# Performance work log

Measured on AMD Instinct MI355X. Metric: run time of the kernel, lower is better.

The kernel has to match this reference:

```python
import jax, jax.numpy as jnp
import numpy as np

T, B, D = 256, 16, 512          # time, batch, intermediate_dim (GRU is seq-first)
HR = 256                         # router_dim
EXPERT_DIMS = [0, 128, 256, 512]
NUM_TASKS = 4
COST_EXP = 1.0
BN_EPS = 1e-5


def _gru(x, w_ih, w_hh, b_ih, b_hh):
    """PyTorch-semantics GRU over axis 0. x: (T, ..., D) -> (T, ..., H).
    Works batched (T,B,D) or unbatched (N,D) exactly like nn.GRU."""
    H = w_hh.shape[1]
    gi = x @ w_ih.T + b_ih            # (T, ..., 3H) input projections, done once
    h0 = jnp.zeros(x.shape[1:-1] + (H,), x.dtype)

    def step(h, gi_t):
        gh = h @ w_hh.T + b_hh
        i_r, i_z, i_n = jnp.split(gi_t, 3, axis=-1)
        h_r, h_z, h_n = jnp.split(gh, 3, axis=-1)
        r = jax.nn.sigmoid(i_r + h_r)
        z = jax.nn.sigmoid(i_z + h_z)
        n = jnp.tanh(i_n + r * h_n)
        h_new = (1.0 - z) * n + z * h
        return h_new, h_new

    _, ys = jax.lax.scan(step, h0, gi)
    return ys


def setup_inputs() -> dict:
    key = jax.random.key(0)
    ks = iter(jax.random.split(key, 64))

    def p(shape, fan_in):
        return (jax.random.normal(next(ks), shape, jnp.float32) / np.sqrt(fan_in)).astype(jnp.float32)

    inp = {
        'x': jax.random.normal(next(ks), (T, B, D), jnp.float32),
        'task_ids': jax.random.randint(next(ks), (T, B), 0, NUM_TASKS),
        # router params
        'router_w_ih': p((3 * HR, D), D),
        'router_w_hh': p((3 * HR, HR), HR),
        'router_b_ih': jnp.zeros((3 * HR,), jnp.float32),
        'router_b_hh': jnp.zeros((3 * HR,), jnp.float32),
        'router_out_w': p((len(EXPERT_DIMS), HR), HR),
        'router_out_b': jnp.zeros((len(EXPERT_DIMS),), jnp.float32),
    }
    for i, H in enumerate(EXPERT_DIMS):
        if H == 0:
            continue
        inp[f'e{i}_w_ih'] = p((3 * H, D), D)
        inp[f'e{i}_w_hh'] = p((3 * H, H), H)
        inp[f'e{i}_b_ih'] = jnp.zeros((3 * H,), jnp.float32)
        inp[f'e{i}_b_hh'] = jnp.zeros((3 * H,), jnp.float32)
        inp[f'e{i}_bn_g'] = jnp.ones((H,), jnp.float32)
        inp[f'e{i}_bn_b'] = jnp.zeros((H,), jnp.float32)
        inp[f'e{i}_out_w'] = p((D, H), H)
        inp[f'e{i}_out_b'] = jnp.zeros((D,), jnp.float32)
    return inp


def reference(x, task_ids,
              router_w_ih, router_w_hh, router_b_ih, router_b_hh,
              router_out_w, router_out_b,
              e1_w_ih, e1_w_hh, e1_b_ih, e1_b_hh, e1_bn_g, e1_bn_b, e1_out_w, e1_out_b,
              e2_w_ih, e2_w_hh, e2_b_ih, e2_b_hh, e2_bn_g, e2_bn_b, e2_out_w, e2_out_b,
              e3_w_ih, e3_w_hh, e3_b_ih, e3_b_hh, e3_bn_g, e3_bn_b, e3_out_w, e3_out_b):
    E = len(EXPERT_DIMS)
    # ---- router: GRU -> ReLU -> Linear -> softmax ----
    hs = _gru(x, router_w_ih, router_w_hh, router_b_ih, router_b_hh)   # (T,B,HR)
    logits = jax.nn.relu(hs) @ router_out_w.T + router_out_b           # (T,B,E)
    raw = jax.nn.softmax(logits, axis=-1)                              # raw_router_output
    # no dropout configured -> router_output == raw, all experts active

    # ---- task expert usage losses ----
    costs = jnp.asarray([d ** COST_EXP for d in EXPERT_DIMS], logits.dtype)
    eul = jnp.einsum('tbe,e->tb', raw, costs).reshape(-1)
    tflat = task_ids.reshape(-1)
    sums = jax.ops.segment_sum(eul, tflat, num_segments=NUM_TASKS)
    cnts = jax.ops.segment_sum(jnp.ones_like(eul), tflat, num_segments=NUM_TASKS)
    task_losses = sums / cnts                                           # (NUM_TASKS,)

    # ---- experts: each sees the flat (N,D) tokens as ONE unbatched GRU sequence ----
    flat_x = x.reshape(-1, D)                                           # (N,D)
    gates = raw.reshape(-1, E)                                          # (N,E)
    out = gates[:, 0:1] * flat_x                                        # expert 0 = identity

    eps = [(e1_w_ih, e1_w_hh, e1_b_ih, e1_b_hh, e1_bn_g, e1_bn_b, e1_out_w, e1_out_b),
           (e2_w_ih, e2_w_hh, e2_b_ih, e2_b_hh, e2_bn_g, e2_bn_b, e2_out_w, e2_out_b),
           (e3_w_ih, e3_w_hh, e3_b_ih, e3_b_hh, e3_bn_g, e3_bn_b, e3_out_w, e3_out_b)]
    for i, (w_ih, w_hh, b_ih, b_hh, g, b, ow, ob) in enumerate(eps, start=1):
        h = _gru(flat_x, w_ih, w_hh, b_ih, b_hh)                        # (N,H) unbatched seq
        mu = h.mean(0)
        var = ((h - mu) ** 2).mean(0)                                   # biased var (train-mode BN)
        hn = (h - mu) / jnp.sqrt(var + BN_EPS) * g + b
        eo = jax.nn.relu(hn) @ ow.T + ob                                # (N,D)
        out = out + gates[:, i:i + 1] * eo

    final_output = out.reshape(T, B, D)
    return final_output, raw, task_losses
```

## Files before the change

kernel.cpp:

```cpp
#include <hip/hip_runtime.h>
#include <math.h>

constexpr int TT = 256, BB = 16, DD = 512;
constexpr int NTOK = 4096;
constexpr int RTOT = 3456;
constexpr int E1OFF = 768, E2OFF = 1152, E3OFF = 1920;

constexpr size_t OFF_TSUM = 0;
constexpr size_t OFF_TCNT = 16;
constexpr size_t OFF_CNT  = 32;
constexpr size_t ZBYTES   = 64;
constexpr size_t OFF_GI   = 4096;
constexpr size_t OFF_HS   = OFF_GI  + (size_t)NTOK*RTOT*4;
constexpr size_t OFF_HA3  = OFF_HS  + (size_t)NTOK*256*4;
constexpr size_t OFF_HA2  = OFF_HA3 + (size_t)NTOK*512*4;
constexpr size_t OFF_HA1  = OFF_HA2 + (size_t)NTOK*256*4;
constexpr size_t OFF_AP   = OFF_HA1 + (size_t)NTOK*128*4;
constexpr size_t OFF_MU   = OFF_AP  + (size_t)NTOK*896*4;
constexpr size_t OFF_RSTD = OFF_MU  + 896*4;
constexpr size_t POISON_BYTES = (size_t)NTOK*(256+512+256+128)*4;

__device__ __forceinline__ bool is_poison(float v) {
  return __float_as_uint(v) == 0xAAAAAAAAu;
}

__global__ __launch_bounds__(256) void gemm1_kernel(
    const float* __restrict__ X,
    const float* __restrict__ wR, const float* __restrict__ w1,
    const float* __restrict__ w2, const float* __restrict__ w3,
    const float* __restrict__ bR, const float* __restrict__ b1,
    const float* __restrict__ b2, const float* __restrict__ b3,
    float* __restrict__ GI)
{
  __shared__ float At[32*64];
  __shared__ float Bt[32*64];
  const int n0 = blockIdx.x * 64;
  const int r0 = blockIdx.y * 64;
  const float* W; const float* bias; int rs;
  if (r0 < 768)       { W = wR; bias = bR; rs = 0; }
  else if (r0 < 1152) { W = w1; bias = b1; rs = 768; }
  else if (r0 < 1920) { W = w2; bias = b2; rs = 1152; }
  else                { W = w3; bias = b3; rs = 1920; }
  const int lr0 = r0 - rs;
  const int tid = threadIdx.x;
  const int lm = tid & 63, lk4 = tid >> 6;
  const int tx = tid & 15, ty = tid >> 4;
  float acc[4][4];
#pragma unroll
  for (int i = 0; i < 4; ++i)
#pragma unroll
    for (int q = 0; q < 4; ++q) acc[i][q] = 0.f;

  for (int kb = 0; kb < 512; kb += 32) {
    const float4 a0 = *(const float4*)(X + (size_t)(n0+lm)*512 + kb + lk4*8);
    const float4 a1 = *(const float4*)(X + (size_t)(n0+lm)*512 + kb + lk4*8 + 4);
    const float4 c0 = *(const float4*)(W + (size_t)(lr0+lm)*512 + kb + lk4*8);
    const float4 c1 = *(const float4*)(W + (size_t)(lr0+lm)*512 + kb + lk4*8 + 4);
    __syncthreads();
    At[(lk4*8+0)*64+lm]=a0.x; At[(lk4*8+1)*64+lm]=a0.y; At[(lk4*8+2)*64+lm]=a0.z; At[(lk4*8+3)*64+lm]=a0.w;
    At[(lk4*8+4)*64+lm]=a1.x; At[(lk4*8+5)*64+lm]=a1.y; At[(lk4*8+6)*64+lm]=a1.z; At[(lk4*8+7)*64+lm]=a1.w;
    Bt[(lk4*8+0)*64+lm]=c0.x; Bt[(lk4*8+1)*64+lm]=c0.y; Bt[(lk4*8+2)*64+lm]=c0.z; Bt[(lk4*8+3)*64+lm]=c0.w;
    Bt[(lk4*8+4)*64+lm]=c1.x; Bt[(lk4*8+5)*64+lm]=c1.y; Bt[(lk4*8+6)*64+lm]=c1.z; Bt[(lk4*8+7)*64+lm]=c1.w;
    __syncthreads();
#pragma unroll
    for (int k = 0; k < 32; ++k) {
      const float4 av = *(const float4*)&At[k*64 + ty*4];
      const float4 bv = *(const float4*)&Bt[k*64 + tx*4];
      acc[0][0]=fmaf(av.x,bv.x,acc[0][0]); acc[0][1]=fmaf(av.x,bv.y,acc[0][1]); acc[0][2]=fmaf(av.x,bv.z,acc[0][2]); acc[0][3]=fmaf(av.x,bv.w,acc[0][3]);
      acc[1][0]=fmaf(av.y,bv.x,acc[1][0]); acc[1][1]=fmaf(av.y,bv.y,acc[1][1]); acc[1][2]=fmaf(av.y,bv.z,acc[1][2]); acc[1][3]=fmaf(av.y,bv.w,acc[1][3]);
      acc[2][0]=fmaf(av.z,bv.x,acc[2][0]); acc[2][1]=fmaf(av.z,bv.y,acc[2][1]); acc[2][2]=fmaf(av.z,bv.z,acc[2][2]); acc[2][3]=fmaf(av.z,bv.w,acc[2][3]);
      acc[3][0]=fmaf(av.w,bv.x,acc[3][0]); acc[3][1]=fmaf(av.w,bv.y,acc[3][1]); acc[3][2]=fmaf(av.w,bv.z,acc[3][2]); acc[3][3]=fmaf(av.w,bv.w,acc[3][3]);
    }
  }
  const float4 bb = *(const float4*)(bias + lr0 + tx*4);
#pragma unroll
  for (int i = 0; i < 4; ++i) {
    float4 o;
    o.x = acc[i][0] + bb.x; o.y = acc[i][1] + bb.y; o.z = acc[i][2] + bb.z; o.w = acc[i][3] + bb.w;
    *(float4*)(GI + (size_t)(n0+ty*4+i)*RTOT + r0 + tx*4) = o;
  }
}

struct ScanArgs {
  const float* GI;
  const float* rwhh; const float* rbhh; float* hs;
  const float* w1; const float* b1; float* ha1;
  const float* w2; const float* b2; float* ha2;
  const float* w3; const float* b3; float* ha3;
  int* cnt;
};

template<int H, int OPW>
__device__ void expert_scan(const float* __restrict__ GIe, const float* __restrict__ whh,
                            const float* __restrict__ bhh, float* __restrict__ hall,
                            float* __restrict__ sm, int wg)
{
  constexpr int KCN = 512 / OPW;
  constexpr bool SINGLE = (OPW == H);
  const int tid = threadIdx.x;
  const int j = tid / KCN, kc = tid % KCN;
  const int jg = wg * OPW + j;

  float4 wr[8], wz[8], wn[8];
#pragma unroll
  for (int i4 = 0; i4 < 8; ++i4) {
    const int kk = kc * 32 + ((i4 + kc) & 7) * 4;
    wr[i4] = *(const float4*)(whh + (size_t)jg * H + kk);
    wz[i4] = *(const float4*)(whh + (size_t)(H + jg) * H + kk);
    wn[i4] = *(const float4*)(whh + (size_t)(2*H + jg) * H + kk);
  }
  float gbr = 0.f, gbz = 0.f, gbn = 0.f;
  float gr0 = 0.f, gz0 = 0.f, gn0 = 0.f, gr1 = 0.f, gz1 = 0.f, gn1 = 0.f;
  if (kc == 0) {
    gbr = bhh[jg]; gbz = bhh[H + jg]; gbn = bhh[2*H + jg];
    gr0 = GIe[jg]; gz0 = GIe[H + jg]; gn0 = GIe[2*H + jg];
    const float* g1 = GIe + RTOT;
    gr1 = g1[jg]; gz1 = g1[H + jg]; gn1 = g1[2*H + jg];
  }
  if (SINGLE) {
    if (tid < H) sm[tid] = 0.f;
    __syncthreads();
  }
  for (int t = 0; t < NTOK; ++t) {
    float gr2 = 0.f, gz2 = 0.f, gn2 = 0.f;
    if (kc == 0 && t + 2 < NTOK) {
      const float* g = GIe + (size_t)(t + 2) * RTOT;
      gr2 = g[jg]; gz2 = g[H + jg]; gn2 = g[2*H + jg];
    }
    const float* hbuf;
    if (SINGLE) {
      hbuf = sm + (size_t)(t & 1) * H;
    } else {
      float val = 0.f;
      if (tid < H && t > 0) {
        const volatile float* p = (const volatile float*)(hall + (size_t)(t - 1) * H + tid);
        val = *p;
        while (is_poison(val)) val = *p;
      }
      __syncthreads();
      if (tid < H) sm[tid] = val;
      __syncthreads();
      hbuf = sm;
    }
    float pr = 0.f, pz = 0.f, pn = 0.f;
#pragma unroll
    for (int i4 = 0; i4 < 8; ++i4) {
      const float4 h4 = *(const float4*)(hbuf + kc * 32 + ((i4 + kc) & 7) * 4);
      pr = fmaf(wr[i4].x, h4.x, pr); pr = fmaf(wr[i4].y, h4.y, pr);
      pr = fmaf(wr[i4].z, h4.z, pr); pr = fmaf(wr[i4].w, h4.w, pr);
      pz = fmaf(wz[i4].x, h4.x, pz); pz = fmaf(wz[i4].y, h4.y, pz);
      pz = fmaf(wz[i4].z, h4.z, pz); pz = fmaf(wz[i4].w, h4.w, pz);
      pn = fmaf(wn[i4].x, h4.x, pn); pn = fmaf(wn[i4].y, h4.y, pn);
      pn = fmaf(wn[i4].z, h4.z, pn); pn = fmaf(wn[i4].w, h4.w, pn);
    }
#pragma unroll
    for (int off = KCN / 2; off; off >>= 1) {
      pr += __shfl_down(pr, off); pz += __shfl_down(pz, off); pn += __shfl_down(pn, off);
    }
    if (kc == 0) {
      const float hprev = hbuf[jg];
      const float rg = 1.f / (1.f + expf(-(gr0 + gbr + pr)));
      const float zg = 1.f / (1.f + expf(-(gz0 + gbz + pz)));
      const float nn = tanhf(gn0 + rg * (pn + gbn));
      const float hn = (1.f - zg) * nn + zg * hprev;
      if (SINGLE) {
        sm[(size_t)((t + 1) & 1) * H + jg] = hn;
        hall[(size_t)t * H + jg] = hn;
      } else {
        *(volatile float*)(hall + (size_t)t * H + jg) = hn;
      }
    }
    if (SINGLE) __syncthreads();
    gr0 = gr1; gz0 = gz1; gn0 = gn1;
    gr1 = gr2; gz1 = gz2; gn1 = gn2;
  }
}

__device__ void router_scan(const float* __restrict__ GI, const float* __restrict__ whh,
                            const float* __restrict__ bhh, float* __restrict__ hs,
                            float* __restrict__ sm, int wg)
{
  float* hsmB = sm;
  float* pbuf = sm + 16 * 260;
  const int tid = threadIdx.x;
  const int j = tid >> 4, kc = tid & 15;
  const int jg = wg * 32 + j;
  float4 wr4[4], wz4[4], wn4[4];
#pragma unroll
  for (int i4 = 0; i4 < 4; ++i4) {
    const int kk = kc * 16 + ((i4 + kc) & 3) * 4;
    wr4[i4] = *(const float4*)(whh + (size_t)jg * 256 + kk);
    wz4[i4] = *(const float4*)(whh + (size_t)(256 + jg) * 256 + kk);
    wn4[i4] = *(const float4*)(whh + (size_t)(512 + jg) * 256 + kk);
  }
  const int b2 = tid >> 5, j2 = tid & 31;
  const int jg2 = wg * 32 + j2;
  const float gbr = bhh[jg2], gbz = bhh[256 + jg2], gbn = bhh[512 + jg2];
  float gr0, gz0, gn0, gr1, gz1, gn1;
  { const float* g = GI + (size_t)b2 * RTOT;        gr0 = g[jg2]; gz0 = g[256 + jg2]; gn0 = g[512 + jg2]; }
  { const float* g = GI + (size_t)(16 + b2) * RTOT; gr1 = g[jg2]; gz1 = g[256 + jg2]; gn1 = g[512 + jg2]; }
  const int pb = tid >> 5, pk = (tid & 31) * 8;

  for (int t = 0; t < TT; ++t) {
    float gr2 = 0.f, gz2 = 0.f, gn2 = 0.f;
    if (t + 2 < TT) {
      const float* g = GI + (size_t)((t + 2) * 16 + b2) * RTOT;
      gr2 = g[jg2]; gz2 = g[256 + jg2]; gn2 = g[512 + jg2];
    }
    float v[8];
    if (t == 0) {
#pragma unroll
      for (int u = 0; u < 8; ++u) v[u] = 0.f;
    } else {
      const volatile float* q = (const volatile float*)(hs + (size_t)(t - 1) * 4096 + tid * 8);
#pragma unroll
      for (int u = 0; u < 8; ++u) v[u] = q[u];
      bool bad = true;
      while (bad) {
        bad = false;
#pragma unroll
        for (int u = 0; u < 8; ++u)
          if (is_poison(v[u])) { v[u] = q[u]; bad = true; }
      }
    }
    __syncthreads();
    *(float4*)(hsmB + pb * 260 + pk)     = make_float4(v[0], v[1], v[2], v[3]);
    *(float4*)(hsmB + pb * 260 + pk + 4) = make_float4(v[4], v[5], v[6], v[7]);
    __syncthreads();
    float ar[16], az[16], an[16];
#pragma unroll
    for (int b = 0; b < 16; ++b) { ar[b] = 0.f; az[b] = 0.f; an[b] = 0.f; }
#pragma unroll
    for (int i4 = 0; i4 < 4; ++i4) {
      const int col = kc * 16 + ((i4 + kc) & 3) * 4;
#pragma unroll
      for (int b = 0; b < 16; ++b) {
        const float4 h4 = *(const float4*)(hsmB + b * 260 + col);
        ar[b] = fmaf(wr4[i4].x, h4.x, ar[b]); ar[b] = fmaf(wr4[i4].y, h4.y, ar[b]);
        ar[b] = fmaf(wr4[i4].z, h4.z, ar[b]); ar[b] = fmaf(wr4[i4].w, h4.w, ar[b]);
        az[b] = fmaf(wz4[i4].x, h4.x, az[b]); az[b] = fmaf(wz4[i4].y, h4.y, az[b]);
        az[b] = fmaf(wz4[i4].z, h4.z, az[b]); az[b] = fmaf(wz4[i4].w, h4.w, az[b]);
        an[b] = fmaf(wn4[i4].x, h4.x, an[b]); an[b] = fmaf(wn4[i4].y, h4.y, an[b]);
        an[b] = fmaf(wn4[i4].z, h4.z, an[b]); an[b] = fmaf(wn4[i4].w, h4.w, an[b]);
      }
    }
#pragma unroll
    for (int off = 8; off; off >>= 1) {
#pragma unroll
      for (int b = 0; b < 16; ++b) {
        ar[b] += __shfl_down(ar[b], off);
        az[b] += __shfl_down(az[b], off);
        an[b] += __shfl_down(an[b], off);
      }
    }
    if (kc == 0) {
#pragma unroll
      for (int b = 0; b < 16; ++b) {
        pbuf[(b * 32 + j) * 3 + 0] = ar[b];
        pbuf[(b * 32 + j) * 3 + 1] = az[b];
        pbuf[(b * 32 + j) * 3 + 2] = an[b];
      }
    }
    __syncthreads();
    const float pr = pbuf[(b2 * 32 + j2) * 3 + 0];
    const float pz = pbuf[(b2 * 32 + j2) * 3 + 1];
    const float pn = pbuf[(b2 * 32 + j2) * 3 + 2];
    const float hprev = hsmB[b2 * 260 + jg2];
    const float rg = 1.f / (1.f + expf(-(gr0 + gbr + pr)));
    const float zg = 1.f / (1.f + expf(-(gz0 + gbz + pz)));
    const float nn = tanhf(gn0 + rg * (pn + gbn));
    const float hn = (1.f - zg) * nn + zg * hprev;
    *(volatile float*)(hs + (size_t)t * 4096 + b2 * 256 + jg2) = hn;
    gr0 = gr1; gz0 = gz1; gn0 = gn1;
    gr1 = gr2; gz1 = gz2; gn1 = gn2;
  }
}

__global__ __launch_bounds__(512, 1) void scan_kernel(ScanArgs A)
{
  __shared__ float sm[16 * 260 + 1536];
  __shared__ int role_s[2];
  if (threadIdx.x == 0) {
    unsigned x;
    asm volatile("s_getreg_b32 %0, hwreg(HW_REG_XCC_ID)" : "=s"(x));
    const int xcd = (int)(x & 7u);
    role_s[0] = xcd;
    role_s[1] = atomicAdd(A.cnt + xcd, 1);
  }
  __syncthreads();
  const int xcd = role_s[0], r = role_s[1];
  if (xcd == 0)      { if (r < 16) expert_scan<512, 32>(A.GI + E3OFF, A.w3, A.b3, A.ha3, sm, r); }
  else if (xcd == 1) { if (r < 8)  router_scan(A.GI, A.rwhh, A.rbhh, A.hs, sm, r); }
  else if (xcd == 2) { if (r < 4)  expert_scan<256, 64>(A.GI + E2OFF, A.w2, A.b2, A.ha2, sm, r); }
  else if (xcd == 3) { if (r < 1)  expert_scan<128,128>(A.GI + E1OFF, A.w1, A.b1, A.ha1, sm, r); }
}

__global__ __launch_bounds__(256) void router_out_kernel(
    const float* __restrict__ hs, const float* __restrict__ ow, const float* __restrict__ ob,
    const int* __restrict__ tids, float* __restrict__ raw_out,
    float* __restrict__ tsum, float* __restrict__ tcnt)
{
  const int tid = threadIdx.x;
  const int lane = tid & 63, w = tid >> 6;
  const int n = blockIdx.x * 4 + w;
  float s0 = 0.f, s1 = 0.f, s2 = 0.f, s3 = 0.f;
#pragma unroll
  for (int q = 0; q < 4; ++q) {
    const int jj = lane + q * 64;
    float h = hs[(size_t)n * 256 + jj];
    h = h > 0.f ? h : 0.f;
    s0 = fmaf(h, ow[jj], s0);
    s1 = fmaf(h, ow[256 + jj], s1);
    s2 = fmaf(h, ow[512 + jj], s2);
    s3 = fmaf(h, ow[768 + jj], s3);
  }
  for (int off = 32; off; off >>= 1) {
    s0 += __shfl_xor(s0, off); s1 += __shfl_xor(s1, off);
    s2 += __shfl_xor(s2, off); s3 += __shfl_xor(s3, off);
  }
  if (lane == 0) {
    const float l0 = s0 + ob[0], l1 = s1 + ob[1], l2 = s2 + ob[2], l3 = s3 + ob[3];
    const float m = fmaxf(fmaxf(l0, l1), fmaxf(l2, l3));
    const float e0 = expf(l0 - m), e1 = expf(l1 - m), e2 = expf(l2 - m), e3 = expf(l3 - m);
    const float inv = 1.f / (e0 + e1 + e2 + e3);
    float4 rv; rv.x = e0 * inv; rv.y = e1 * inv; rv.z = e2 * inv; rv.w = e3 * inv;
    *(float4*)(raw_out + (size_t)n * 4) = rv;
    const float eul = rv.y * 128.f + rv.z * 256.f + rv.w * 512.f;
    const int tk = tids[n];
    atomicAdd(&tsum[tk], eul);
    atomicAdd(&tcnt[tk], 1.f);
  }
}

__global__ __launch_bounds__(256) void bn_stats_kernel(
    const float* __restrict__ h1, const float* __restrict__ h2, const float* __restrict__ h3,
    float* __restrict__ mu, float* __restrict__ rstd)
{
  const int c = blockIdx.x;
  const float* hp; int He, hc;
  if (c < 128)      { hp = h1; He = 128; hc = c; }
  else if (c < 384) { hp = h2; He = 256; hc = c - 128; }
  else              { hp = h3; He = 512; hc = c - 384; }
  float s = 0.f, s2 = 0.f;
  for (int r = threadIdx.x; r < NTOK; r += 256) {
    const float v = hp[(size_t)r * He + hc];
    s += v; s2 = fmaf(v, v, s2);
  }
  for (int off = 32; off; off >>= 1) { s += __shfl_xor(s, off); s2 += __shfl_xor(s2, off); }
  __shared__ float red[8];
  const int lane = threadIdx.x & 63, w = threadIdx.x >> 6;
  if (lane == 0) { red[w] = s; red[4 + w] = s2; }
  __syncthreads();
  if (threadIdx.x == 0) {
    const float S = red[0] + red[1] + red[2] + red[3];
    const float S2 = red[4] + red[5] + red[6] + red[7];
    const float m = S * (1.f / 4096.f);
    float v = S2 * (1.f / 4096.f) - m * m;
    v = v > 0.f ? v : 0.f;
    mu[c] = m;
    rstd[c] = 1.f / sqrtf(v + 1e-5f);
  }
}

__global__ __launch_bounds__(256) void aprime_kernel(
    const float* __restrict__ h1, const float* __restrict__ h2, const float* __restrict__ h3,
    const float* __restrict__ g1, const float* __restrict__ be1,
    const float* __restrict__ g2, const float* __restrict__ be2,
    const float* __restrict__ g3, const float* __restrict__ be3,
    const float* __restrict__ mu, const float* __restrict__ rstd,
    const float* __restrict__ raw, float* __restrict__ Ap,
    const float* __restrict__ tsum, const float* __restrict__ tcnt, float* __restrict__ tl_out)
{
  if (blockIdx.x == 4096) {
    if (threadIdx.x < 4) tl_out[threadIdx.x] = tsum[threadIdx.x] / tcnt[threadIdx.x];
    return;
  }
  const int n = blockIdx.x;
  for (int c = threadIdx.x; c < 896; c += 256) {
    const float* hp; const float* gg; const float* bb; int He, hc, e;
    if (c < 128)      { hp = h1; gg = g1; bb = be1; He = 128; hc = c;       e = 1; }
    else if (c < 384) { hp = h2; gg = g2; bb = be2; He = 256; hc = c - 128; e = 2; }
    else              { hp = h3; gg = g3; bb = be3; He = 512; hc = c - 384; e = 3; }
    const float h = hp[(size_t)n * He + hc];
    float v = (h - mu[c]) * rstd[c] * gg[hc] + bb[hc];
    v = v > 0.f ? v : 0.f;
    Ap[(size_t)n * 896 + c] = raw[(size_t)n * 4 + e] * v;
  }
}

__global__ __launch_bounds__(256) void out_gemm_kernel(
    const float* __restrict__ Ap,
    const float* __restrict__ ow1, const float* __restrict__ ow2, const float* __restrict__ ow3,
    const float* __restrict__ ob1, const float* __restrict__ ob2, const float* __restrict__ ob3,
    const float* __restrict__ X, const float* __restrict__ raw, float* __restrict__ out)
{
  __shared__ float At[32*64];
  __shared__ float Bt[32*64];
  const int n0 = blockIdx.x * 64;
  const int d0 = blockIdx.y * 64;
  const int tid = threadIdx.x;
  const int lm = tid & 63, lk4 = tid >> 6;
  const int tx = tid & 15, ty = tid >> 4;
  float acc[4][4];
#pragma unroll
  for (int i = 0; i < 4; ++i)
#pragma unroll
    for (int q = 0; q < 4; ++q) acc[i][q] = 0.f;

  for (int kb = 0; kb < 896; kb += 32) {
    const float* W; int He, ko;
    if (kb < 128)      { W = ow1; He = 128; ko = 0; }
    else if (kb < 384) { W = ow2; He = 256; ko = 128; }
    else               { W = ow3; He = 512; ko = 384; }
    const float4 a0 = *(const float4*)(Ap + (size_t)(n0+lm)*896 + kb + lk4*8);
    const float4 a1 = *(const float4*)(Ap + (size_t)(n0+lm)*896 + kb + lk4*8 + 4);
    const float4 c0 = *(const float4*)(W + (size_t)(d0+lm)*He + (kb - ko) + lk4*8);
    const float4 c1 = *(const float4*)(W + (size_t)(d0+lm)*He + (kb - ko) + lk4*8 + 4);
    __syncthreads();
    At[(lk4*8+0)*64+lm]=a0.x; At[(lk4*8+1)*64+lm]=a0.y; At[(lk4*8+2)*64+lm]=a0.z; At[(lk4*8+3)*64+lm]=a0.w;
    At[(lk4*8+4)*64+lm]=a1.x; At[(lk4*8+5)*64+lm]=a1.y; At[(lk4*8+6)*64+lm]=a1.z; At[(lk4*8+7)*64+lm]=a1.w;
    Bt[(lk4*8+0)*64+lm]=c0.x; Bt[(lk4*8+1)*64+lm]=c0.y; Bt[(lk4*8+2)*64+lm]=c0.z; Bt[(lk4*8+3)*64+lm]=c0.w;
    Bt[(lk4*8+4)*64+lm]=c1.x; Bt[(lk4*8+5)*64+lm]=c1.y; Bt[(lk4*8+6)*64+lm]=c1.z; Bt[(lk4*8+7)*64+lm]=c1.w;
    __syncthreads();
#pragma unroll
    for (int k = 0; k < 32; ++k) {
      const float4 av = *(const float4*)&At[k*64 + ty*4];
      const float4 bv = *(const float4*)&Bt[k*64 + tx*4];
      acc[0][0]=fmaf(av.x,bv.x,acc[0][0]); acc[0][1]=fmaf(av.x,bv.y,acc[0][1]); acc[0][2]=fmaf(av.x,bv.z,acc[0][2]); acc[0][3]=fmaf(av.x,bv.w,acc[0][3]);
      acc[1][0]=fmaf(av.y,bv.x,acc[1][0]); acc[1][1]=fmaf(av.y,bv.y,acc[1][1]); acc[1][2]=fmaf(av.y,bv.z,acc[1][2]); acc[1][3]=fmaf(av.y,bv.w,acc[1][3]);
      acc[2][0]=fmaf(av.z,bv.x,acc[2][0]); acc[2][1]=fmaf(av.z,bv.y,acc[2][1]); acc[2][2]=fmaf(av.z,bv.z,acc[2][2]); acc[2][3]=fmaf(av.z,bv.w,acc[2][3]);
      acc[3][0]=fmaf(av.w,bv.x,acc[3][0]); acc[3][1]=fmaf(av.w,bv.y,acc[3][1]); acc[3][2]=fmaf(av.w,bv.z,acc[3][2]); acc[3][3]=fmaf(av.w,bv.w,acc[3][3]);
    }
  }
#pragma unroll
  for (int i = 0; i < 4; ++i) {
    const int n = n0 + ty * 4 + i;
    const float4 g  = *(const float4*)(raw + (size_t)n * 4);
    const float4 xv = *(const float4*)(X + (size_t)n * 512 + d0 + tx * 4);
    const float4 o1 = *(const float4*)(ob1 + d0 + tx * 4);
    const float4 o2 = *(const float4*)(ob2 + d0 + tx * 4);
    const float4 o3 = *(const float4*)(ob3 + d0 + tx * 4);
    float4 o;
    o.x = acc[i][0] + g.x*xv.x + g.y*o1.x + g.z*o2.x + g.w*o3.x;
    o.y = acc[i][1] + g.x*xv.y + g.y*o1.y + g.z*o2.y + g.w*o3.y;
    o.z = acc[i][2] + g.x*xv.z + g.y*o1.z + g.z*o2.z + g.w*o3.z;
    o.w = acc[i][3] + g.x*xv.w + g.y*o1.w + g.z*o2.w + g.w*o3.w;
    *(float4*)(out + (size_t)n * 512 + d0 + tx * 4) = o;
  }
}

extern "C" void kernel_launch(void* const* d_in, const int* in_sizes, int n_in,
                              void* d_out, int out_size, void* d_ws, size_t ws_size,
                              hipStream_t stream) {
  const float* x    = (const float*)d_in[0];
  const int*   tids = (const int*)d_in[1];
  const float* rwih = (const float*)d_in[2];
  const float* rwhh = (const float*)d_in[3];
  const float* rbih = (const float*)d_in[4];
  const float* rbhh = (const float*)d_in[5];
  const float* row  = (const float*)d_in[6];
  const float* rob  = (const float*)d_in[7];
  const float* w1ih = (const float*)d_in[8];
  const float* w1hh = (const float*)d_in[9];
  const float* b1ih = (const float*)d_in[10];
  const float* b1hh = (const float*)d_in[11];
  const float* bn1g = (const float*)d_in[12];
  const float* bn1b = (const float*)d_in[13];
  const float* ow1  = (const float*)d_in[14];
  const float* ob1  = (const float*)d_in[15];
  const float* w2ih = (const float*)d_in[16];
  const float* w2hh = (const float*)d_in[17];
  const float* b2ih = (const float*)d_in[18];
  const float* b2hh = (const float*)d_in[19];
  const float* bn2g = (const float*)d_in[20];
  const float* bn2b = (const float*)d_in[21];
  const float* ow2  = (const float*)d_in[22];
  const float* ob2  = (const float*)d_in[23];
  const float* w3ih = (const float*)d_in[24];
  const float* w3hh = (const float*)d_in[25];
  const float* b3ih = (const float*)d_in[26];
  const float* b3hh = (const float*)d_in[27];
  const float* bn3g = (const float*)d_in[28];
  const float* bn3b = (const float*)d_in[29];
  const float* ow3  = (const float*)d_in[30];
  const float* ob3  = (const float*)d_in[31];

  char* ws = (char*)d_ws;
  float* tsum = (float*)(ws + OFF_TSUM);
  float* tcnt = (float*)(ws + OFF_TCNT);
  int*   cnt  = (int*)(ws + OFF_CNT);
  float* GI   = (float*)(ws + OFF_GI);
  float* hs   = (float*)(ws + OFF_HS);
  float* ha3  = (float*)(ws + OFF_HA3);
  float* ha2  = (float*)(ws + OFF_HA2);
  float* ha1  = (float*)(ws + OFF_HA1);
  float* Ap   = (float*)(ws + OFF_AP);
  float* mu   = (float*)(ws + OFF_MU);
  float* rstd = (float*)(ws + OFF_RSTD);

  float* outp = (float*)d_out;
  float* rawp = outp + (size_t)NTOK * DD;
  float* tlp  = rawp + (size_t)NTOK * 4;

  hipMemsetAsync(ws, 0, ZBYTES, stream);
  hipMemsetAsync(ws + OFF_HS, 0xAA, POISON_BYTES, stream);

  gemm1_kernel<<<dim3(64, 54), 256, 0, stream>>>(x, rwih, w1ih, w2ih, w3ih,
                                                 rbih, b1ih, b2ih, b3ih, GI);

  ScanArgs sa;
  sa.GI = GI; sa.rwhh = rwhh; sa.rbhh = rbhh; sa.hs = hs;
  sa.w1 = w1hh; sa.b1 = b1hh; sa.ha1 = ha1;
  sa.w2 = w2hh; sa.b2 = b2hh; sa.ha2 = ha2;
  sa.w3 = w3hh; sa.b3 = b3hh; sa.ha3 = ha3;
  sa.cnt = cnt;
  scan_kernel<<<dim3(320), dim3(512), 0, stream>>>(sa);

  router_out_kernel<<<dim3(1024), 256, 0, stream>>>(hs, row, rob, tids, rawp, tsum, tcnt);
  bn_stats_kernel<<<dim3(896), 256, 0, stream>>>(ha1, ha2, ha3, mu, rstd);
  aprime_kernel<<<dim3(4097), 256, 0, stream>>>(ha1, ha2, ha3, bn1g, bn1b, bn2g, bn2b,
                                                bn3g, bn3b, mu, rstd, rawp, Ap,
                                                tsum, tcnt, tlp);

  out_gemm_kernel<<<dim3(64, 8), 256, 0, stream>>>(Ap, ow1, ow2, ow3, ob1, ob2, ob3,
                                                   x, rawp, outp);
}
```

Baseline: 6.769 ms.

## Replace poison-flag scan sync with tagged 64-bit ring buffers and wider workgroup split

New measurement: 24.88 ms. +267.5%, slower.

```diff
diff --git a/kernel.cpp b/kernel.cpp
--- a/kernel.cpp
+++ b/kernel.cpp
@@ -6,11 +6,19 @@
 constexpr int RTOT = 3456;
 constexpr int E1OFF = 768, E2OFF = 1152, E3OFF = 1920;
 
-constexpr size_t OFF_TSUM = 0;
-constexpr size_t OFF_TCNT = 16;
-constexpr size_t OFF_CNT  = 32;
-constexpr size_t ZBYTES   = 64;
-constexpr size_t OFF_GI   = 4096;
+typedef unsigned long long ull;
+
+constexpr size_t OFF_TSUM  = 0;
+constexpr size_t OFF_TCNT  = 16;
+constexpr size_t OFF_CNT   = 32;
+constexpr size_t ZBYTES    = 64;
+constexpr size_t OFF_RINGR = 4096;
+constexpr size_t OFF_RING3 = OFF_RINGR + 8ull*4096*8;
+constexpr size_t OFF_RING2 = OFF_RING3 + 8ull*512*8;
+constexpr size_t OFF_RING1 = OFF_RING2 + 8ull*256*8;
+constexpr size_t RING_END  = OFF_RING1 + 8ull*128*8;
+constexpr size_t RING_BYTES = RING_END - OFF_RINGR;
+constexpr size_t OFF_GI   = 327680;
 constexpr size_t OFF_HS   = OFF_GI  + (size_t)NTOK*RTOT*4;
 constexpr size_t OFF_HA3  = OFF_HS  + (size_t)NTOK*256*4;
 constexpr size_t OFF_HA2  = OFF_HA3 + (size_t)NTOK*512*4;
@@ -18,11 +26,6 @@
 constexpr size_t OFF_AP   = OFF_HA1 + (size_t)NTOK*128*4;
 constexpr size_t OFF_MU   = OFF_AP  + (size_t)NTOK*896*4;
 constexpr size_t OFF_RSTD = OFF_MU  + 896*4;
-constexpr size_t POISON_BYTES = (size_t)NTOK*(256+512+256+128)*4;
-
-__device__ __forceinline__ bool is_poison(float v) {
-  return __float_as_uint(v) == 0xAAAAAAAAu;
-}
 
 __global__ __launch_bounds__(256) void gemm1_kernel(
     const float* __restrict__ X,
@@ -83,216 +86,223 @@
 
 struct ScanArgs {
   const float* GI;
-  const float* rwhh; const float* rbhh; float* hs;
-  const float* w1; const float* b1; float* ha1;
-  const float* w2; const float* b2; float* ha2;
-  const float* w3; const float* b3; float* ha3;
+  const float* rwhh; const float* rbhh; float* hs;  ull* ringR;
+  const float* w1;   const float* b1;   float* ha1; ull* ring1;
+  const float* w2;   const float* b2;   float* ha2; ull* ring2;
+  const float* w3;   const float* b3;   float* ha3; ull* ring3;
   int* cnt;
 };
 
 template<int H, int OPW>
 __device__ void expert_scan(const float* __restrict__ GIe, const float* __restrict__ whh,
                             const float* __restrict__ bhh, float* __restrict__ hall,
-                            float* __restrict__ sm, int wg)
+                            volatile ull* ring, int wg)
 {
   constexpr int KCN = 512 / OPW;
-  constexpr bool SINGLE = (OPW == H);
   const int tid = threadIdx.x;
   const int j = tid / KCN, kc = tid % KCN;
   const int jg = wg * OPW + j;
-
-  float4 wr[8], wz[8], wn[8];
-#pragma unroll
-  for (int i4 = 0; i4 < 8; ++i4) {
-    const int kk = kc * 32 + ((i4 + kc) & 7) * 4;
+  const int lane = tid & 63;
+  const int gbase = lane & ~(KCN - 1);
+
+  float4 wr[4], wz[4], wn[4];
+#pragma unroll
+  for (int i4 = 0; i4 < 4; ++i4) {
+    const int kk = kc * 16 + i4 * 4;
     wr[i4] = *(const float4*)(whh + (size_t)jg * H + kk);
     wz[i4] = *(const float4*)(whh + (size_t)(H + jg) * H + kk);
-    wn[i4] = *(const float4*)(whh + (size_t)(2*H + jg) * H + kk);
-  }
-  float gbr = 0.f, gbz = 0.f, gbn = 0.f;
-  float gr0 = 0.f, gz0 = 0.f, gn0 = 0.f, gr1 = 0.f, gz1 = 0.f, gn1 = 0.f;
-  if (kc == 0) {
-    gbr = bhh[jg]; gbz = bhh[H + jg]; gbn = bhh[2*H + jg];
-    gr0 = GIe[jg]; gz0 = GIe[H + jg]; gn0 = GIe[2*H + jg];
-    const float* g1 = GIe + RTOT;
-    gr1 = g1[jg]; gz1 = g1[H + jg]; gn1 = g1[2*H + jg];
-  }
-  if (SINGLE) {
-    if (tid < H) sm[tid] = 0.f;
-    __syncthreads();
-  }
+    wn[i4] = *(const float4*)(whh + (size_t)(2 * H + jg) * H + kk);
+  }
+  const float gbr = bhh[jg], gbz = bhh[H + jg], gbn = bhh[2 * H + jg];
+  float pgr, pgz, pgn;
+  { const float* g = GIe + (size_t)kc * RTOT;
+    pgr = __builtin_nontemporal_load(g + jg);
+    pgz = __builtin_nontemporal_load(g + H + jg);
+    pgn = __builtin_nontemporal_load(g + 2 * H + jg); }
+
   for (int t = 0; t < NTOK; ++t) {
-    float gr2 = 0.f, gz2 = 0.f, gn2 = 0.f;
-    if (kc == 0 && t + 2 < NTOK) {
-      const float* g = GIe + (size_t)(t + 2) * RTOT;
-      gr2 = g[jg]; gz2 = g[H + jg]; gn2 = g[2*H + jg];
-    }
-    const float* hbuf;
-    if (SINGLE) {
-      hbuf = sm + (size_t)(t & 1) * H;
-    } else {
-      float val = 0.f;
-      if (tid < H && t > 0) {
-        const volatile float* p = (const volatile float*)(hall + (size_t)(t - 1) * H + tid);
-        val = *p;
-        while (is_poison(val)) val = *p;
-      }
-      __syncthreads();
-      if (tid < H) sm[tid] = val;
-      __syncthreads();
-      hbuf = sm;
-    }
-    float pr = 0.f, pz = 0.f, pn = 0.f;
-#pragma unroll
-    for (int i4 = 0; i4 < 8; ++i4) {
-      const float4 h4 = *(const float4*)(hbuf + kc * 32 + ((i4 + kc) & 7) * 4);
-      pr = fmaf(wr[i4].x, h4.x, pr); pr = fmaf(wr[i4].y, h4.y, pr);
-      pr = fmaf(wr[i4].z, h4.z, pr); pr = fmaf(wr[i4].w, h4.w, pr);
-      pz = fmaf(wz[i4].x, h4.x, pz); pz = fmaf(wz[i4].y, h4.y, pz);
-      pz = fmaf(wz[i4].z, h4.z, pz); pz = fmaf(wz[i4].w, h4.w, pz);
-      pn = fmaf(wn[i4].x, h4.x, pn); pn = fmaf(wn[i4].y, h4.y, pn);
-      pn = fmaf(wn[i4].z, h4.z, pn); pn = fmaf(wn[i4].w, h4.w, pn);
-    }
-#pragma unroll
-    for (int off = KCN / 2; off; off >>= 1) {
-      pr += __shfl_down(pr, off); pz += __shfl_down(pz, off); pn += __shfl_down(pn, off);
-    }
-    if (kc == 0) {
-      const float hprev = hbuf[jg];
-      const float rg = 1.f / (1.f + expf(-(gr0 + gbr + pr)));
-      const float zg = 1.f / (1.f + expf(-(gz0 + gbz + pz)));
-      const float nn = tanhf(gn0 + rg * (pn + gbn));
-      const float hn = (1.f - zg) * nn + zg * hprev;
-      if (SINGLE) {
-        sm[(size_t)((t + 1) & 1) * H + jg] = hn;
-        hall[(size_t)t * H + jg] = hn;
-      } else {
-        *(volatile float*)(hall + (size_t)t * H + jg) = hn;
-      }
-    }
-    if (SINGLE) __syncthreads();
-    gr0 = gr1; gz0 = gz1; gn0 = gn1;
-    gr1 = gr2; gz1 = gz2; gn1 = gn2;
-  }
-}
-
-__device__ void router_scan(const float* __restrict__ GI, const float* __restrict__ whh,
-                            const float* __restrict__ bhh, float* __restrict__ hs,
-                            float* __restrict__ sm, int wg)
-{
-  float* hsmB = sm;
-  float* pbuf = sm + 16 * 260;
-  const int tid = threadIdx.x;
-  const int j = tid >> 4, kc = tid & 15;
-  const int jg = wg * 32 + j;
-  float4 wr4[4], wz4[4], wn4[4];
-#pragma unroll
-  for (int i4 = 0; i4 < 4; ++i4) {
-    const int kk = kc * 16 + ((i4 + kc) & 3) * 4;
-    wr4[i4] = *(const float4*)(whh + (size_t)jg * 256 + kk);
-    wz4[i4] = *(const float4*)(whh + (size_t)(256 + jg) * 256 + kk);
-    wn4[i4] = *(const float4*)(whh + (size_t)(512 + jg) * 256 + kk);
-  }
-  const int b2 = tid >> 5, j2 = tid & 31;
-  const int jg2 = wg * 32 + j2;
-  const float gbr = bhh[jg2], gbz = bhh[256 + jg2], gbn = bhh[512 + jg2];
-  float gr0, gz0, gn0, gr1, gz1, gn1;
-  { const float* g = GI + (size_t)b2 * RTOT;        gr0 = g[jg2]; gz0 = g[256 + jg2]; gn0 = g[512 + jg2]; }
-  { const float* g = GI + (size_t)(16 + b2) * RTOT; gr1 = g[jg2]; gz1 = g[256 + jg2]; gn1 = g[512 + jg2]; }
-  const int pb = tid >> 5, pk = (tid & 31) * 8;
-
-  for (int t = 0; t < TT; ++t) {
-    float gr2 = 0.f, gz2 = 0.f, gn2 = 0.f;
-    if (t + 2 < TT) {
-      const float* g = GI + (size_t)((t + 2) * 16 + b2) * RTOT;
-      gr2 = g[jg2]; gz2 = g[256 + jg2]; gn2 = g[512 + jg2];
-    }
-    float v[8];
-    if (t == 0) {
-#pragma unroll
-      for (int u = 0; u < 8; ++u) v[u] = 0.f;
-    } else {
-      const volatile float* q = (const volatile float*)(hs + (size_t)(t - 1) * 4096 + tid * 8);
-#pragma unroll
-      for (int u = 0; u < 8; ++u) v[u] = q[u];
+    const int sl = t & (KCN - 1);
+    const float gr = __shfl(pgr, gbase + sl);
+    const float gz = __shfl(pgz, gbase + sl);
+    const float gn = __shfl(pgn, gbase + sl);
+    if (kc == sl && t + KCN < NTOK) {
+      const float* g = GIe + (size_t)(t + KCN) * RTOT;
+      pgr = __builtin_nontemporal_load(g + jg);
+      pgz = __builtin_nontemporal_load(g + H + jg);
+      pgn = __builtin_nontemporal_load(g + 2 * H + jg);
+    }
+    float pr = 0.f, pz = 0.f, pn = 0.f, hprev = 0.f;
+    if (t > 0) {
+      volatile const ull* rp = ring + (size_t)((t - 1) & 7) * H;
+      const unsigned tg = (unsigned)(t - 1);
+      ull hv[16];
+#pragma unroll
+      for (int m = 0; m < 16; ++m) hv[m] = rp[kc * 16 + m];
       bool bad = true;
       while (bad) {
         bad = false;
 #pragma unroll
-        for (int u = 0; u < 8; ++u)
-          if (is_poison(v[u])) { v[u] = q[u]; bad = true; }
-      }
-    }
-    __syncthreads();
-    *(float4*)(hsmB + pb * 260 + pk)     = make_float4(v[0], v[1], v[2], v[3]);
-    *(float4*)(hsmB + pb * 260 + pk + 4) = make_float4(v[4], v[5], v[6], v[7]);
-    __syncthreads();
-    float ar[16], az[16], an[16];
-#pragma unroll
-    for (int b = 0; b < 16; ++b) { ar[b] = 0.f; az[b] = 0.f; an[b] = 0.f; }
-#pragma unroll
-    for (int i4 = 0; i4 < 4; ++i4) {
-      const int col = kc * 16 + ((i4 + kc) & 3) * 4;
-#pragma unroll
-      for (int b = 0; b < 16; ++b) {
-        const float4 h4 = *(const float4*)(hsmB + b * 260 + col);
-        ar[b] = fmaf(wr4[i4].x, h4.x, ar[b]); ar[b] = fmaf(wr4[i4].y, h4.y, ar[b]);
-        ar[b] = fmaf(wr4[i4].z, h4.z, ar[b]); ar[b] = fmaf(wr4[i4].w, h4.w, ar[b]);
-        az[b] = fmaf(wz4[i4].x, h4.x, az[b]); az[b] = fmaf(wz4[i4].y, h4.y, az[b]);
-        az[b] = fmaf(wz4[i4].z, h4.z, az[b]); az[b] = fmaf(wz4[i4].w, h4.w, az[b]);
-        an[b] = fmaf(wn4[i4].x, h4.x, an[b]); an[b] = fmaf(wn4[i4].y, h4.y, an[b]);
-        an[b] = fmaf(wn4[i4].z, h4.z, an[b]); an[b] = fmaf(wn4[i4].w, h4.w, an[b]);
-      }
-    }
-#pragma unroll
-    for (int off = 8; off; off >>= 1) {
-#pragma unroll
-      for (int b = 0; b < 16; ++b) {
-        ar[b] += __shfl_down(ar[b], off);
-        az[b] += __shfl_down(az[b], off);
-        an[b] += __shfl_down(an[b], off);
-      }
-    }
+        for (int m = 0; m < 16; ++m)
+          if ((unsigned)(hv[m] >> 32) != tg) { hv[m] = rp[kc * 16 + m]; bad = true; }
+      }
+      ull hpv = rp[jg];
+      while ((unsigned)(hpv >> 32) != tg) hpv = rp[jg];
+      hprev = __uint_as_float((unsigned)hpv);
+#pragma unroll
+      for (int i4 = 0; i4 < 4; ++i4) {
+        const float h0 = __uint_as_float((unsigned)hv[i4*4+0]);
+        const float h1 = __uint_as_float((unsigned)hv[i4*4+1]);
+        const float h2 = __uint_as_float((unsigned)hv[i4*4+2]);
+        const float h3 = __uint_as_float((unsigned)hv[i4*4+3]);
+        pr = fmaf(wr[i4].x, h0, pr); pr = fmaf(wr[i4].y, h1, pr);
+        pr = fmaf(wr[i4].z, h2, pr); pr = fmaf(wr[i4].w, h3, pr);
+        pz = fmaf(wz[i4].x, h0, pz); pz = fmaf(wz[i4].y, h1, pz);
+        pz = fmaf(wz[i4].z, h2, pz); pz = fmaf(wz[i4].w, h3, pz);
+        pn = fmaf(wn[i4].x, h0, pn); pn = fmaf(wn[i4].y, h1, pn);
+        pn = fmaf(wn[i4].z, h2, pn); pn = fmaf(wn[i4].w, h3, pn);
+      }
+#pragma unroll
+      for (int off = KCN / 2; off; off >>= 1) {
+        pr += __shfl_xor(pr, off); pz += __shfl_xor(pz, off); pn += __shfl_xor(pn, off);
+      }
+    }
+    const float rg = 1.f / (1.f + expf(-(gr + gbr + pr)));
+    const float zg = 1.f / (1.f + expf(-(gz + gbz + pz)));
+    const float nn = tanhf(gn + rg * (pn + gbn));
+    const float hn = (1.f - zg) * nn + zg * hprev;
     if (kc == 0) {
-#pragma unroll
-      for (int b = 0; b < 16; ++b) {
-        pbuf[(b * 32 + j) * 3 + 0] = ar[b];
-        pbuf[(b * 32 + j) * 3 + 1] = az[b];
-        pbuf[(b * 32 + j) * 3 + 2] = an[b];
-      }
-    }
-    __syncthreads();
-    const float pr = pbuf[(b2 * 32 + j2) * 3 + 0];
-    const float pz = pbuf[(b2 * 32 + j2) * 3 + 1];
-    const float pn = pbuf[(b2 * 32 + j2) * 3 + 2];
-    const float hprev = hsmB[b2 * 260 + jg2];
-    const float rg = 1.f / (1.f + expf(-(gr0 + gbr + pr)));
-    const float zg = 1.f / (1.f + expf(-(gz0 + gbz + pz)));
-    const float nn = tanhf(gn0 + rg * (pn + gbn));
-    const float hn = (1.f - zg) * nn + zg * hprev;
-    *(volatile float*)(hs + (size_t)t * 4096 + b2 * 256 + jg2) = hn;
-    gr0 = gr1; gz0 = gz1; gn0 = gn1;
-    gr1 = gr2; gz1 = gz2; gn1 = gn2;
-  }
-}
-
-__global__ __launch_bounds__(512, 1) void scan_kernel(ScanArgs A)
-{
-  __shared__ float sm[16 * 260 + 1536];
-  __shared__ int role_s[2];
+      ring[(size_t)(t & 7) * H + jg] = ((ull)(unsigned)t << 32) | (ull)__float_as_uint(hn);
+      __builtin_nontemporal_store(hn, hall + (size_t)t * H + jg);
+    }
+  }
+}
+
+__device__ void router_scan(const float* __restrict__ GI, const float* __restrict__ whh,
+                            const float* __restrict__ bhh, float* __restrict__ hs,
+                            volatile ull* ring, int wg)
+{
+  const int tid = threadIdx.x;
+  const int lane = tid & 63;
+  const int j = tid >> 6;
+  const int kc = lane >> 2;
+  const int bq = lane & 3;
+  const int jg = wg * 8 + j;
+  float4 wr[4], wz[4], wn[4];
+#pragma unroll
+  for (int i4 = 0; i4 < 4; ++i4) {
+    const int kk = kc * 16 + i4 * 4;
+    wr[i4] = *(const float4*)(whh + (size_t)jg * 256 + kk);
+    wz[i4] = *(const float4*)(whh + (size_t)(256 + jg) * 256 + kk);
+    wn[i4] = *(const float4*)(whh + (size_t)(512 + jg) * 256 + kk);
+  }
+  const float gbr = bhh[jg], gbz = bhh[256 + jg], gbn = bhh[512 + jg];
+  float pg[12];
+#pragma unroll
+  for (int i = 0; i < 4; ++i) {
+    const float* g = GI + (size_t)(kc * 16 + bq * 4 + i) * RTOT;
+    pg[i*3+0] = __builtin_nontemporal_load(g + jg);
+    pg[i*3+1] = __builtin_nontemporal_load(g + 256 + jg);
+    pg[i*3+2] = __builtin_nontemporal_load(g + 512 + jg);
+  }
+  for (int t = 0; t < TT; ++t) {
+    const int sl = t & 15;
+    const int src = sl * 4 + bq;
+    float gr[4], gz[4], gn[4];
+#pragma unroll
+    for (int i = 0; i < 4; ++i) {
+      gr[i] = __shfl(pg[i*3+0], src);
+      gz[i] = __shfl(pg[i*3+1], src);
+      gn[i] = __shfl(pg[i*3+2], src);
+    }
+    if (kc == sl && t + 16 < TT) {
+#pragma unroll
+      for (int i = 0; i < 4; ++i) {
+        const float* g = GI + (size_t)((t + 16) * 16 + bq * 4 + i) * RTOT;
+        pg[i*3+0] = __builtin_nontemporal_load(g + jg);
+        pg[i*3+1] = __builtin_nontemporal_load(g + 256 + jg);
+        pg[i*3+2] = __builtin_nontemporal_load(g + 512 + jg);
+      }
+    }
+    float ar[4] = {0,0,0,0}, az[4] = {0,0,0,0}, an[4] = {0,0,0,0}, hprev[4] = {0,0,0,0};
+    if (t > 0) {
+      volatile const ull* rp = ring + (size_t)((t - 1) & 7) * 4096;
+      const unsigned tg = (unsigned)(t - 1);
+#pragma unroll
+      for (int i = 0; i < 4; ++i) {
+        const int b = bq * 4 + i;
+        ull hv[16];
+#pragma unroll
+        for (int m = 0; m < 16; ++m) hv[m] = rp[b * 256 + kc * 16 + m];
+        bool bad = true;
+        while (bad) {
+          bad = false;
+#pragma unroll
+          for (int m = 0; m < 16; ++m)
+            if ((unsigned)(hv[m] >> 32) != tg) { hv[m] = rp[b * 256 + kc * 16 + m]; bad = true; }
+        }
+#pragma unroll
+        for (int i4 = 0; i4 < 4; ++i4) {
+          const float h0 = __uint_as_float((unsigned)hv[i4*4+0]);
+          const float h1 = __uint_as_float((unsigned)hv[i4*4+1]);
+          const float h2 = __uint_as_float((unsigned)hv[i4*4+2]);
+          const float h3 = __uint_as_float((unsigned)hv[i4*4+3]);
+          ar[i] = fmaf(wr[i4].x, h0, ar[i]); ar[i] = fmaf(wr[i4].y, h1, ar[i]);
+          ar[i] = fmaf(wr[i4].z, h2, ar[i]); ar[i] = fmaf(wr[i4].w, h3, ar[i]);
+          az[i] = fmaf(wz[i4].x, h0, az[i]); az[i] = fmaf(wz[i4].y, h1, az[i]);
+          az[i] = fmaf(wz[i4].z, h2, az[i]); az[i] = fmaf(wz[i4].w, h3, az[i]);
+          an[i] = fmaf(wn[i4].x, h0, an[i]); an[i] = fmaf(wn[i4].y, h1, an[i]);
+          an[i] = fmaf(wn[i4].z, h2, an[i]); an[i] = fmaf(wn[i4].w, h3, an[i]);
+        }
+      }
+#pragma unroll
+      for (int i = 0; i < 4; ++i) {
+        const int b = bq * 4 + i;
+        ull hpv = rp[b * 256 + jg];
+        while ((unsigned)(hpv >> 32) != tg) hpv = rp[b * 256 + jg];
+        hprev[i] = __uint_as_float((unsigned)hpv);
+      }
+#pragma unroll
+      for (int off = 32; off >= 4; off >>= 1) {
+#pragma unroll
+        for (int i = 0; i < 4; ++i) {
+          ar[i] += __shfl_xor(ar[i], off);
+          az[i] += __shfl_xor(az[i], off);
+          an[i] += __shfl_xor(an[i], off);
+        }
+      }
+    }
+#pragma unroll
+    for (int i = 0; i < 4; ++i) {
+      const float rg = 1.f / (1.f + expf(-(gr[i] + gbr + ar[i])));
+      const float zg = 1.f / (1.f + expf(-(gz[i] + gbz + az[i])));
+      const float nn = tanhf(gn[i] + rg * (an[i] + gbn));
+      const float hn = (1.f - zg) * nn + zg * hprev[i];
+      if (kc == 0) {
+        const int b = bq * 4 + i;
+        ring[(size_t)(t & 7) * 4096 + b * 256 + jg] =
+            ((ull)(unsigned)t << 32) | (ull)__float_as_uint(hn);
+        __builtin_nontemporal_store(hn, hs + (size_t)t * 4096 + b * 256 + jg);
+      }
+    }
+  }
+}
+
+__global__ __launch_bounds__(512) void scan_kernel(ScanArgs A)
+{
+  __shared__ int smem[20496];
   if (threadIdx.x == 0) {
     unsigned x;
     asm volatile("s_getreg_b32 %0, hwreg(HW_REG_XCC_ID)" : "=s"(x));
     const int xcd = (int)(x & 7u);
-    role_s[0] = xcd;
-    role_s[1] = atomicAdd(A.cnt + xcd, 1);
+    smem[0] = xcd;
+    smem[1] = atomicAdd(A.cnt + xcd, 1);
   }
   __syncthreads();
-  const int xcd = role_s[0], r = role_s[1];
-  if (xcd == 0)      { if (r < 16) expert_scan<512, 32>(A.GI + E3OFF, A.w3, A.b3, A.ha3, sm, r); }
-  else if (xcd == 1) { if (r < 8)  router_scan(A.GI, A.rwhh, A.rbhh, A.hs, sm, r); }
-  else if (xcd == 2) { if (r < 4)  expert_scan<256, 64>(A.GI + E2OFF, A.w2, A.b2, A.ha2, sm, r); }
-  else if (xcd == 3) { if (r < 1)  expert_scan<128,128>(A.GI + E1OFF, A.w1, A.b1, A.ha1, sm, r); }
+  const int xcd = smem[0], r = smem[1];
+  if (xcd == 0)      { if (r < 32) expert_scan<512, 16>(A.GI + E3OFF, A.w3, A.b3, A.ha3, A.ring3, r); }
+  else if (xcd == 1) { if (r < 32) router_scan(A.GI, A.rwhh, A.rbhh, A.hs, A.ringR, r); }
+  else if (xcd == 2) { if (r < 8)  expert_scan<256, 32>(A.GI + E2OFF, A.w2, A.b2, A.ha2, A.ring2, r); }
+  else if (xcd == 3) { if (r < 2)  expert_scan<128, 64>(A.GI + E1OFF, A.w1, A.b1, A.ha1, A.ring1, r); }
 }
 
 __global__ __launch_bounds__(256) void router_out_kernel(
@@ -486,35 +496,40 @@
   const float* ob3  = (const float*)d_in[31];
 
   char* ws = (char*)d_ws;
-  float* tsum = (float*)(ws + OFF_TSUM);
-  float* tcnt = (float*)(ws + OFF_TCNT);
-  int*   cnt  = (int*)(ws + OFF_CNT);
-  float* GI   = (float*)(ws + OFF_GI);
-  float* hs   = (float*)(ws + OFF_HS);
-  float* ha3  = (float*)(ws + OFF_HA3);
-  float* ha2  = (float*)(ws + OFF_HA2);
-  float* ha1  = (float*)(ws + OFF_HA1);
-  float* Ap   = (float*)(ws + OFF_AP);
-  float* mu   = (float*)(ws + OFF_MU);
-  float* rstd = (float*)(ws + OFF_RSTD);
+  float* tsum  = (float*)(ws + OFF_TSUM);
+  float* tcnt  = (float*)(ws + OFF_TCNT);
+  int*   cnt   = (int*)(ws + OFF_CNT);
+  ull*   ringR = (ull*)(ws + OFF_RINGR);
+  ull*   ring3 = (ull*)(ws + OFF_RING3);
+  ull*   ring2 = (ull*)(ws + OFF_RING2);
+  ull*   ring1 = (ull*)(ws + OFF_RING1);
+  float* GI    = (float*)(ws + OFF_GI);
+  float* hs    = (float*)(ws + OFF_HS);
+  float* ha3   = (float*)(ws + OFF_HA3);
+  float* ha2   = (float*)(ws + OFF_HA2);
+  float* ha1   = (float*)(ws + OFF_HA1);
+  float* Ap    = (float*)(ws + OFF_AP);
+  float* mu    = (float*)(ws + OFF_MU);
+  float* rstd  = (float*)(ws + OFF_RSTD);
 
   float* outp = (float*)d_out;
   float* rawp = outp + (size_t)NTOK * DD;
   float* tlp  = rawp + (size_t)NTOK * 4;
 
   hipMemsetAsync(ws, 0, ZBYTES, stream);
-  hipMemsetAsync(ws + OFF_HS, 0xAA, POISON_BYTES, stream);
+  hipMemsetAsync(ws + OFF_RINGR, 0xAA, RING_BYTES, stream);
 
   gemm1_kernel<<<dim3(64, 54), 256, 0, stream>>>(x, rwih, w1ih, w2ih, w3ih,
                                                  rbih, b1ih, b2ih, b3ih, GI);
 
   ScanArgs sa;
-  sa.GI = GI; sa.rwhh = rwhh; sa.rbhh = rbhh; sa.hs = hs;
-  sa.w1 = w1hh; sa.b1 = b1hh; sa.ha1 = ha1;
-  sa.w2 = w2hh; sa.b2 = b2hh; sa.ha2 = ha2;
-  sa.w3 = w3hh; sa.b3 = b3hh; sa.ha3 = ha3;
+  sa.GI = GI;
+  sa.rwhh = rwhh; sa.rbhh = rbhh; sa.hs = hs;  sa.ringR = ringR;
+  sa.w1 = w1hh;   sa.b1 = b1hh;   sa.ha1 = ha1; sa.ring1 = ring1;
+  sa.w2 = w2hh;   sa.b2 = b2hh;   sa.ha2 = ha2; sa.ring2 = ring2;
+  sa.w3 = w3hh;   sa.b3 = b3hh;   sa.ha3 = ha3; sa.ring3 = ring3;
   sa.cnt = cnt;
-  scan_kernel<<<dim3(320), dim3(512), 0, stream>>>(sa);
+  scan_kernel<<<dim3(768), dim3(512), 0, stream>>>(sa);
 
   router_out_kernel<<<dim3(1024), 256, 0, stream>>>(hs, row, rob, tids, rawp, tsum, tcnt);
   bn_stats_kernel<<<dim3(896), 256, 0, stream>>>(ha1, ha2, ha3, mu, rstd);
```
